# Kernel optimization log

Measured on AMD Instinct MI355X. Metric: run time of the kernel, lower is better.

## Reference

```python
import jax, jax.numpy as jnp
import numpy as np

NEG_BIG = -9.0e15


def masked_mean_softmax(idx):
    # softmax over a 0/-inf mask == uniform weights over positions where idx > 0
    logits = jnp.where(idx > 0, 1.0, NEG_BIG).astype(jnp.float32)
    return jax.nn.softmax(logits, axis=1)


def setup_inputs() -> dict:
    key = jax.random.key(0)
    ks = jax.random.split(key, 8)
    N_NODES, N_EDGES, EDGE_ARITY, NODE_DEG = 100000, 50000, 32, 16
    D_IN, D_OUT, TV = 128, 128, 128
    stdv = 1.0 / np.sqrt(D_IN)
    u = lambda k, shp: jax.random.uniform(k, shp, jnp.float32, -stdv, stdv)
    return {
        "x": jax.random.normal(ks[0], (N_NODES, D_IN), jnp.float32),
        "seq": jax.random.randint(ks[1], (N_EDGES, EDGE_ARITY), 0, N_NODES),
        "useq": jax.random.randint(ks[2], (N_NODES, NODE_DEG), 0, N_EDGES),
        "TextVector": jax.random.normal(ks[3], (TV,), jnp.float32),
        "weight1": u(ks[4], (D_IN, D_OUT)),
        "weight2": u(ks[5], (D_OUT, D_OUT)),
        "weight3": u(ks[6], (TV, TV)),
    }


def reference(x, seq, useq, TextVector, weight1, weight2, weight3):
    # NOTE: the torch module overwrites TextVector with weight3[0]; dropout is
    # a no-op in eval mode and is omitted here.
    tv = weight3[0]                                   # [TV]
    dot = weight3 @ tv                                # [TV]
    cos = dot / (jnp.linalg.norm(tv) * jnp.linalg.norm(weight3, axis=1))
    inter_nw = jnp.mean(cos)                          # scalar

    xw = (x @ weight1) * inter_nw                     # [N, D_OUT]

    nor = masked_mean_softmax(seq)                    # [E, A]
    adj_with_fea = xw[seq]                            # [E, A, D_OUT] gather
    edge = jnp.einsum('eac,ea->ec', adj_with_fea, nor)
    edge = jax.nn.relu(edge)
    e1 = edge @ weight2                               # [E, D_OUT]

    u_nor = masked_mean_softmax(useq)                 # [N, K]
    edge_adj = e1[useq]                               # [N, K, D_OUT] gather
    node = jnp.einsum('nkc,nk->nc', edge_adj, u_nor)  # [N, D_OUT]
    return node
```

## Files before the change

### kernel.cpp

```cpp
#include <hip/hip_runtime.h>
#include <hip/hip_fp16.h>

#define ND 100000
#define NE 50000
#define AR 32
#define DG 16
#define D  128

__global__ __launch_bounds__(128) void k_inter(const float* __restrict__ w3,
                                               float* __restrict__ inter_out) {
    int j = threadIdx.x;
    float dot = 0.f, sq = 0.f, sq0 = 0.f;
    #pragma unroll 8
    for (int k = 0; k < D; ++k) {
        float wj = w3[j * D + k];
        float w0 = w3[k];
        dot += wj * w0;
        sq  += wj * wj;
        sq0 += w0 * w0;
    }
    float cosj = dot / (sqrtf(sq0) * sqrtf(sq));
    __shared__ float red[128];
    red[j] = cosj;
    __syncthreads();
    if (j == 0) {
        float s = 0.f;
        for (int i = 0; i < 128; ++i) s += red[i];
        inter_out[0] = s / 128.f;
    }
}

__global__ __launch_bounds__(256) void k_xw(const float* __restrict__ x,
                                            const float* __restrict__ w1,
                                            const float* __restrict__ inter_p,
                                            __half* __restrict__ xwh) {
    __shared__ __half w1h[D * D];
    __shared__ float  xs[32 * D];
    int t = threadIdx.x;

    const float4* w1v4 = (const float4*)w1;
    #pragma unroll
    for (int i = 0; i < 16; ++i) {
        float4 v = w1v4[i * 256 + t];
        __half2* dh = (__half2*)&w1h[(i * 256 + t) * 4];
        dh[0] = __floats2half2_rn(v.x, v.y);
        dh[1] = __floats2half2_rn(v.z, v.w);
    }
    int rowbase = blockIdx.x * 32;
    const float4* xg = (const float4*)(x + (size_t)rowbase * D);
    float4* xs4 = (float4*)xs;
    #pragma unroll
    for (int i = 0; i < 4; ++i) xs4[i * 256 + t] = xg[i * 256 + t];
    __syncthreads();

    float inter = inter_p[0];
    int rg = t >> 5;
    int cg = t & 31;
    int r0 = rg * 4;
    int c0 = cg * 4;

    float acc[4][4] = {};
    #pragma unroll 4
    for (int k = 0; k < D; ++k) {
        float xv[4];
        #pragma unroll
        for (int i = 0; i < 4; ++i) xv[i] = xs[(r0 + i) * D + k];
        __half2 wa = *(const __half2*)&w1h[k * D + c0];
        __half2 wb = *(const __half2*)&w1h[k * D + c0 + 2];
        float wc0 = __low2float(wa), wc1 = __high2float(wa);
        float wc2 = __low2float(wb), wc3 = __high2float(wb);
        #pragma unroll
        for (int i = 0; i < 4; ++i) {
            acc[i][0] = fmaf(xv[i], wc0, acc[i][0]);
            acc[i][1] = fmaf(xv[i], wc1, acc[i][1]);
            acc[i][2] = fmaf(xv[i], wc2, acc[i][2]);
            acc[i][3] = fmaf(xv[i], wc3, acc[i][3]);
        }
    }
    #pragma unroll
    for (int i = 0; i < 4; ++i) {
        size_t r = (size_t)(rowbase + r0 + i);
        __half2* dst = (__half2*)(xwh + r * D + c0);
        dst[0] = __floats2half2_rn(acc[i][0] * inter, acc[i][1] * inter);
        dst[1] = __floats2half2_rn(acc[i][2] * inter, acc[i][3] * inter);
    }
}

__global__ __launch_bounds__(256) void k_edge(const int* __restrict__ seq,
                                              const __half* __restrict__ xwh,
                                              const float* __restrict__ w2,
                                              __half* __restrict__ e1h) {
    __shared__ __half w2h[D * D];
    __shared__ float  ebuf[8][D];
    int t = threadIdx.x;

    const float4* w2v4 = (const float4*)w2;
    #pragma unroll
    for (int i = 0; i < 16; ++i) {
        float4 v = w2v4[i * 256 + t];
        __half2* dh = (__half2*)&w2h[(i * 256 + t) * 4];
        dh[0] = __floats2half2_rn(v.x, v.y);
        dh[1] = __floats2half2_rn(v.z, v.w);
    }

    int wave = t >> 6;
    int lane = t & 63;
    int sub  = lane >> 5;
    int il   = lane & 31;
    int gw   = blockIdx.x * 4 + wave;
    int e    = gw * 2 + sub;

    int  sval  = seq[(size_t)e * AR + il];
    bool valid = sval > 0;
    unsigned long long b = __ballot(valid);
    int cnt = __popcll(sub ? (b >> 32) : (b & 0xffffffffULL));
    const float wuni = 1.f / 32.f;
    float wv = (cnt > 0) ? 1.f / (float)cnt : wuni;

    int c0 = il * 4;
    float a0 = 0.f, a1 = 0.f, a2 = 0.f, a3 = 0.f;
    #pragma unroll
    for (int a = 0; a < AR; ++a) {
        int srow = __shfl(sval, (sub << 5) + a, 64);
        float wa = (cnt > 0) ? ((srow > 0) ? wv : 0.f) : wuni;
        const __half2* p = (const __half2*)(xwh + (size_t)srow * D + c0);
        __half2 v01 = p[0], v23 = p[1];
        a0 = fmaf(wa, __low2float(v01),  a0);
        a1 = fmaf(wa, __high2float(v01), a1);
        a2 = fmaf(wa, __low2float(v23),  a2);
        a3 = fmaf(wa, __high2float(v23), a3);
    }
    float* eb = ebuf[wave * 2 + sub];
    eb[c0 + 0] = fmaxf(a0, 0.f);
    eb[c0 + 1] = fmaxf(a1, 0.f);
    eb[c0 + 2] = fmaxf(a2, 0.f);
    eb[c0 + 3] = fmaxf(a3, 0.f);
    __syncthreads();

    float o0 = 0.f, o1 = 0.f, o2 = 0.f, o3 = 0.f;
    #pragma unroll 4
    for (int c = 0; c < D; ++c) {
        float ec = eb[c];
        __half2 wa2 = *(const __half2*)&w2h[c * D + c0];
        __half2 wb2 = *(const __half2*)&w2h[c * D + c0 + 2];
        o0 = fmaf(ec, __low2float(wa2),  o0);
        o1 = fmaf(ec, __high2float(wa2), o1);
        o2 = fmaf(ec, __low2float(wb2),  o2);
        o3 = fmaf(ec, __high2float(wb2), o3);
    }
    __half2* dst = (__half2*)(e1h + (size_t)e * D + c0);
    dst[0] = __floats2half2_rn(o0, o1);
    dst[1] = __floats2half2_rn(o2, o3);
}

__global__ __launch_bounds__(256) void k_node(const int* __restrict__ useq,
                                              const __half* __restrict__ e1h,
                                              float* __restrict__ out) {
    int t = threadIdx.x;
    int wave = t >> 6, lane = t & 63;
    int n = blockIdx.x * 4 + wave;

    int  sval  = useq[(size_t)n * DG + (lane & 15)];
    bool valid = sval > 0;
    unsigned long long b = __ballot(valid);
    int cnt = __popcll(b & 0xFFFFULL);
    const float wuni = 1.f / 16.f;
    float wv = (cnt > 0) ? 1.f / (float)cnt : wuni;

    float a0 = 0.f, a1 = 0.f;
    #pragma unroll
    for (int k = 0; k < DG; ++k) {
        int srow = __shfl(sval, k, 64);
        float wa = (cnt > 0) ? ((srow > 0) ? wv : 0.f) : wuni;
        __half2 v = *(const __half2*)(e1h + (size_t)srow * D + lane * 2);
        a0 = fmaf(wa, __low2float(v),  a0);
        a1 = fmaf(wa, __high2float(v), a1);
    }
    float2* dst = (float2*)(out + (size_t)n * D + lane * 2);
    *dst = make_float2(a0, a1);
}

extern "C" void kernel_launch(void* const* d_in, const int* in_sizes, int n_in,
                              void* d_out, int out_size, void* d_ws, size_t ws_size,
                              hipStream_t stream) {
    const float* x    = (const float*)d_in[0];
    const int*   seq  = (const int*)d_in[1];
    const int*   useq = (const int*)d_in[2];
    const float* w1   = (const float*)d_in[4];
    const float* w2   = (const float*)d_in[5];
    const float* w3   = (const float*)d_in[6];
    float* out = (float*)d_out;

    __half* xwh   = (__half*)d_out;
    float*  inter = (float*)d_ws;
    __half* e1h   = (__half*)((char*)d_ws + 256);

    hipLaunchKernelGGL(k_inter, dim3(1),       dim3(128), 0, stream, w3, inter);
    hipLaunchKernelGGL(k_xw,    dim3(ND / 32), dim3(256), 0, stream, x, w1, inter, xwh);
    hipLaunchKernelGGL(k_edge,  dim3(NE / 8),  dim3(256), 0, stream, seq, xwh, w2, e1h);
    hipLaunchKernelGGL(k_node,  dim3(ND / 4),  dim3(256), 0, stream, useq, e1h, out);
}
```

Baseline: 269.2 us.

## Use MFMA f16 matrix cores for both dense GEMMs with pre-swizzled weight fragments

Adds a prep kernel that converts w1 and w2 to fp16 and lays them out in MFMA B-fragment order. The x@w1 and edge@w2 products now use mfma_f32_16x16x32_f16 instead of scalar FMA loops, with x also rounded to fp16 in padded shared memory. k_edge now handles 32 edges per block to feed the MFMA tiles. k_node is reworked to load 8 bytes per lane across two half-waves and combine them with a shuffle. This cuts ALU time in the GEMM stages and per-block weight conversion work, at the cost of extra fp16 rounding of x and of the edge activations.

```diff
diff --git a/kernel.cpp b/kernel.cpp
--- a/kernel.cpp
+++ b/kernel.cpp
@@ -6,6 +6,12 @@
 #define AR 32
 #define DG 16
 #define D  128
+
+typedef _Float16 half8_t __attribute__((ext_vector_type(8)));
+typedef _Float16 half4_t __attribute__((ext_vector_type(4)));
+typedef float    f32x4_t __attribute__((ext_vector_type(4)));
+
+#define APAD 136
 
 __global__ __launch_bounds__(128) void k_inter(const float* __restrict__ w3,
                                                float* __restrict__ inter_out) {
@@ -30,154 +36,185 @@
     }
 }
 
+__global__ __launch_bounds__(256) void k_prep(const float* __restrict__ w1,
+                                              const float* __restrict__ w2,
+                                              _Float16* __restrict__ w1f,
+                                              _Float16* __restrict__ w2f) {
+    int o = blockIdx.x * 256 + threadIdx.x;
+    int j    = o & 7;
+    int lane = (o >> 3) & 63;
+    int frag = o >> 9;
+    int ntile = frag >> 2, ktile = frag & 3;
+    int n = ntile * 16 + (lane & 15);
+    int k = ktile * 32 + (lane >> 4) * 8 + j;
+    w1f[o] = (_Float16)w1[k * D + n];
+    w2f[o] = (_Float16)w2[k * D + n];
+}
+
 __global__ __launch_bounds__(256) void k_xw(const float* __restrict__ x,
-                                            const float* __restrict__ w1,
+                                            const _Float16* __restrict__ w1f_g,
                                             const float* __restrict__ inter_p,
-                                            __half* __restrict__ xwh) {
-    __shared__ __half w1h[D * D];
-    __shared__ float  xs[32 * D];
+                                            _Float16* __restrict__ xwh) {
+    __shared__ _Float16 wfrag[D * D];
+    __shared__ _Float16 xs[64 * APAD];
     int t = threadIdx.x;
 
-    const float4* w1v4 = (const float4*)w1;
-    #pragma unroll
-    for (int i = 0; i < 16; ++i) {
-        float4 v = w1v4[i * 256 + t];
-        __half2* dh = (__half2*)&w1h[(i * 256 + t) * 4];
-        dh[0] = __floats2half2_rn(v.x, v.y);
-        dh[1] = __floats2half2_rn(v.z, v.w);
-    }
-    int rowbase = blockIdx.x * 32;
-    const float4* xg = (const float4*)(x + (size_t)rowbase * D);
-    float4* xs4 = (float4*)xs;
-    #pragma unroll
-    for (int i = 0; i < 4; ++i) xs4[i * 256 + t] = xg[i * 256 + t];
+    {
+        const float4* src = (const float4*)w1f_g;
+        float4* dst = (float4*)wfrag;
+        #pragma unroll
+        for (int i = 0; i < 8; ++i) dst[i * 256 + t] = src[i * 256 + t];
+    }
+    int rowbase = blockIdx.x * 64;
+    #pragma unroll
+    for (int p = 0; p < 8; ++p) {
+        int idx = p * 1024 + t * 4;
+        int r = idx >> 7, c = idx & 127;
+        int grow = rowbase + r;
+        float4 v = make_float4(0.f, 0.f, 0.f, 0.f);
+        if (grow < ND) v = ((const float4*)x)[(size_t)grow * 32 + (c >> 2)];
+        half4_t h = { (_Float16)v.x, (_Float16)v.y, (_Float16)v.z, (_Float16)v.w };
+        *(half4_t*)&xs[r * APAD + c] = h;
+    }
     __syncthreads();
 
+    int wave = t >> 6, lane = t & 63;
+    int quad = lane >> 4, l15 = lane & 15;
+    int m0 = wave * 16;
     float inter = inter_p[0];
-    int rg = t >> 5;
-    int cg = t & 31;
-    int r0 = rg * 4;
-    int c0 = cg * 4;
-
-    float acc[4][4] = {};
-    #pragma unroll 4
-    for (int k = 0; k < D; ++k) {
-        float xv[4];
-        #pragma unroll
-        for (int i = 0; i < 4; ++i) xv[i] = xs[(r0 + i) * D + k];
-        __half2 wa = *(const __half2*)&w1h[k * D + c0];
-        __half2 wb = *(const __half2*)&w1h[k * D + c0 + 2];
-        float wc0 = __low2float(wa), wc1 = __high2float(wa);
-        float wc2 = __low2float(wb), wc3 = __high2float(wb);
+
+    half8_t a[4];
+    #pragma unroll
+    for (int kt = 0; kt < 4; ++kt)
+        a[kt] = *(const half8_t*)&xs[(m0 + l15) * APAD + kt * 32 + quad * 8];
+
+    #pragma unroll
+    for (int nt = 0; nt < 8; ++nt) {
+        f32x4_t acc = {0.f, 0.f, 0.f, 0.f};
+        #pragma unroll
+        for (int kt = 0; kt < 4; ++kt) {
+            half8_t b = *(const half8_t*)&wfrag[((nt * 4 + kt) * 64 + lane) * 8];
+            acc = __builtin_amdgcn_mfma_f32_16x16x32_f16(a[kt], b, acc, 0, 0, 0);
+        }
+        int col = nt * 16 + l15;
         #pragma unroll
         for (int i = 0; i < 4; ++i) {
-            acc[i][0] = fmaf(xv[i], wc0, acc[i][0]);
-            acc[i][1] = fmaf(xv[i], wc1, acc[i][1]);
-            acc[i][2] = fmaf(xv[i], wc2, acc[i][2]);
-            acc[i][3] = fmaf(xv[i], wc3, acc[i][3]);
-        }
-    }
-    #pragma unroll
-    for (int i = 0; i < 4; ++i) {
-        size_t r = (size_t)(rowbase + r0 + i);
-        __half2* dst = (__half2*)(xwh + r * D + c0);
-        dst[0] = __floats2half2_rn(acc[i][0] * inter, acc[i][1] * inter);
-        dst[1] = __floats2half2_rn(acc[i][2] * inter, acc[i][3] * inter);
+            int grow = rowbase + m0 + quad * 4 + i;
+            if (grow < ND)
+                xwh[(size_t)grow * D + col] = (_Float16)(acc[i] * inter);
+        }
     }
 }
 
 __global__ __launch_bounds__(256) void k_edge(const int* __restrict__ seq,
-                                              const __half* __restrict__ xwh,
-                                              const float* __restrict__ w2,
-                                              __half* __restrict__ e1h) {
-    __shared__ __half w2h[D * D];
-    __shared__ float  ebuf[8][D];
+                                              const _Float16* __restrict__ xwh,
+                                              const _Float16* __restrict__ w2f_g,
+                                              _Float16* __restrict__ e1h) {
+    __shared__ _Float16 wfrag[D * D];
+    __shared__ _Float16 et[32 * APAD];
     int t = threadIdx.x;
-
-    const float4* w2v4 = (const float4*)w2;
-    #pragma unroll
-    for (int i = 0; i < 16; ++i) {
-        float4 v = w2v4[i * 256 + t];
-        __half2* dh = (__half2*)&w2h[(i * 256 + t) * 4];
-        dh[0] = __floats2half2_rn(v.x, v.y);
-        dh[1] = __floats2half2_rn(v.z, v.w);
-    }
-
-    int wave = t >> 6;
-    int lane = t & 63;
-    int sub  = lane >> 5;
-    int il   = lane & 31;
-    int gw   = blockIdx.x * 4 + wave;
-    int e    = gw * 2 + sub;
-
-    int  sval  = seq[(size_t)e * AR + il];
-    bool valid = sval > 0;
-    unsigned long long b = __ballot(valid);
-    int cnt = __popcll(sub ? (b >> 32) : (b & 0xffffffffULL));
-    const float wuni = 1.f / 32.f;
-    float wv = (cnt > 0) ? 1.f / (float)cnt : wuni;
-
-    int c0 = il * 4;
-    float a0 = 0.f, a1 = 0.f, a2 = 0.f, a3 = 0.f;
-    #pragma unroll
-    for (int a = 0; a < AR; ++a) {
-        int srow = __shfl(sval, (sub << 5) + a, 64);
-        float wa = (cnt > 0) ? ((srow > 0) ? wv : 0.f) : wuni;
-        const __half2* p = (const __half2*)(xwh + (size_t)srow * D + c0);
-        __half2 v01 = p[0], v23 = p[1];
-        a0 = fmaf(wa, __low2float(v01),  a0);
-        a1 = fmaf(wa, __high2float(v01), a1);
-        a2 = fmaf(wa, __low2float(v23),  a2);
-        a3 = fmaf(wa, __high2float(v23), a3);
-    }
-    float* eb = ebuf[wave * 2 + sub];
-    eb[c0 + 0] = fmaxf(a0, 0.f);
-    eb[c0 + 1] = fmaxf(a1, 0.f);
-    eb[c0 + 2] = fmaxf(a2, 0.f);
-    eb[c0 + 3] = fmaxf(a3, 0.f);
+    {
+        const float4* src = (const float4*)w2f_g;
+        float4* dst = (float4*)wfrag;
+        #pragma unroll
+        for (int i = 0; i < 8; ++i) dst[i * 256 + t] = src[i * 256 + t];
+    }
+
+    int wave = t >> 6, lane = t & 63;
+    int sub = lane >> 5, il = lane & 31;
+    int eb0 = blockIdx.x * 32;
+
+    #pragma unroll
+    for (int p = 0; p < 4; ++p) {
+        int erow = p * 8 + wave * 2 + sub;
+        int e = eb0 + erow;
+        int es = (e < NE) ? e : (NE - 1);
+        int sval = seq[(size_t)es * AR + il];
+        unsigned long long b = __ballot(sval > 0);
+        int cnt = __popcll(sub ? (unsigned long long)(b >> 32)
+                               : (b & 0xffffffffULL));
+        const float wuni = 1.f / 32.f;
+        float wv = (cnt > 0) ? 1.f / (float)cnt : wuni;
+        int c0 = il * 4;
+        float a0 = 0.f, a1 = 0.f, a2 = 0.f, a3 = 0.f;
+        #pragma unroll
+        for (int a = 0; a < AR; ++a) {
+            int srow = __shfl(sval, (sub << 5) + a, 64);
+            float wa = (cnt > 0) ? ((srow > 0) ? wv : 0.f) : wuni;
+            half4_t v = *(const half4_t*)(xwh + (size_t)srow * D + c0);
+            a0 = fmaf(wa, (float)v[0], a0);
+            a1 = fmaf(wa, (float)v[1], a1);
+            a2 = fmaf(wa, (float)v[2], a2);
+            a3 = fmaf(wa, (float)v[3], a3);
+        }
+        half4_t h = { (_Float16)fmaxf(a0, 0.f), (_Float16)fmaxf(a1, 0.f),
+                      (_Float16)fmaxf(a2, 0.f), (_Float16)fmaxf(a3, 0.f) };
+        *(half4_t*)&et[erow * APAD + c0] = h;
+    }
     __syncthreads();
 
-    float o0 = 0.f, o1 = 0.f, o2 = 0.f, o3 = 0.f;
-    #pragma unroll 4
-    for (int c = 0; c < D; ++c) {
-        float ec = eb[c];
-        __half2 wa2 = *(const __half2*)&w2h[c * D + c0];
-        __half2 wb2 = *(const __half2*)&w2h[c * D + c0 + 2];
-        o0 = fmaf(ec, __low2float(wa2),  o0);
-        o1 = fmaf(ec, __high2float(wa2), o1);
-        o2 = fmaf(ec, __low2float(wb2),  o2);
-        o3 = fmaf(ec, __high2float(wb2), o3);
-    }
-    __half2* dst = (__half2*)(e1h + (size_t)e * D + c0);
-    dst[0] = __floats2half2_rn(o0, o1);
-    dst[1] = __floats2half2_rn(o2, o3);
+    int quad = lane >> 4, l15 = lane & 15;
+    int m0 = (wave >> 1) * 16;
+    int ng = (wave & 1) * 4;
+
+    half8_t a[4];
+    #pragma unroll
+    for (int kt = 0; kt < 4; ++kt)
+        a[kt] = *(const half8_t*)&et[(m0 + l15) * APAD + kt * 32 + quad * 8];
+
+    #pragma unroll
+    for (int nt2 = 0; nt2 < 4; ++nt2) {
+        int nt = ng + nt2;
+        f32x4_t acc = {0.f, 0.f, 0.f, 0.f};
+        #pragma unroll
+        for (int kt = 0; kt < 4; ++kt) {
+            half8_t b = *(const half8_t*)&wfrag[((nt * 4 + kt) * 64 + lane) * 8];
+            acc = __builtin_amdgcn_mfma_f32_16x16x32_f16(a[kt], b, acc, 0, 0, 0);
+        }
+        int col = nt * 16 + l15;
+        #pragma unroll
+        for (int i = 0; i < 4; ++i) {
+            int e = eb0 + m0 + quad * 4 + i;
+            if (e < NE)
+                e1h[(size_t)e * D + col] = (_Float16)acc[i];
+        }
+    }
 }
 
 __global__ __launch_bounds__(256) void k_node(const int* __restrict__ useq,
-                                              const __half* __restrict__ e1h,
+                                              const _Float16* __restrict__ e1h,
                                               float* __restrict__ out) {
     int t = threadIdx.x;
     int wave = t >> 6, lane = t & 63;
     int n = blockIdx.x * 4 + wave;
-
-    int  sval  = useq[(size_t)n * DG + (lane & 15)];
-    bool valid = sval > 0;
-    unsigned long long b = __ballot(valid);
+    int hf = lane >> 5, il = lane & 31;
+
+    int sval = useq[(size_t)n * DG + (lane & 15)];
+    unsigned long long b = __ballot(sval > 0);
     int cnt = __popcll(b & 0xFFFFULL);
     const float wuni = 1.f / 16.f;
     float wv = (cnt > 0) ? 1.f / (float)cnt : wuni;
 
-    float a0 = 0.f, a1 = 0.f;
-    #pragma unroll
-    for (int k = 0; k < DG; ++k) {
+    float a0 = 0.f, a1 = 0.f, a2 = 0.f, a3 = 0.f;
+    #pragma unroll
+    for (int i = 0; i < 8; ++i) {
+        int k = i * 2 + hf;
         int srow = __shfl(sval, k, 64);
         float wa = (cnt > 0) ? ((srow > 0) ? wv : 0.f) : wuni;
-        __half2 v = *(const __half2*)(e1h + (size_t)srow * D + lane * 2);
-        a0 = fmaf(wa, __low2float(v),  a0);
-        a1 = fmaf(wa, __high2float(v), a1);
-    }
-    float2* dst = (float2*)(out + (size_t)n * D + lane * 2);
-    *dst = make_float2(a0, a1);
+        half4_t v = *(const half4_t*)(e1h + (size_t)srow * D + il * 4);
+        a0 = fmaf(wa, (float)v[0], a0);
+        a1 = fmaf(wa, (float)v[1], a1);
+        a2 = fmaf(wa, (float)v[2], a2);
+        a3 = fmaf(wa, (float)v[3], a3);
+    }
+    a0 += __shfl_down(a0, 32, 64);
+    a1 += __shfl_down(a1, 32, 64);
+    a2 += __shfl_down(a2, 32, 64);
+    a3 += __shfl_down(a3, 32, 64);
+    if (lane < 32) {
+        float4 o = make_float4(a0, a1, a2, a3);
+        ((float4*)(out + (size_t)n * D))[il] = o;
+    }
 }
 
 extern "C" void kernel_launch(void* const* d_in, const int* in_sizes, int n_in,
@@ -191,12 +228,15 @@
     const float* w3   = (const float*)d_in[6];
     float* out = (float*)d_out;
 
-    __half* xwh   = (__half*)d_out;
-    float*  inter = (float*)d_ws;
-    __half* e1h   = (__half*)((char*)d_ws + 256);
-
-    hipLaunchKernelGGL(k_inter, dim3(1),       dim3(128), 0, stream, w3, inter);
-    hipLaunchKernelGGL(k_xw,    dim3(ND / 32), dim3(256), 0, stream, x, w1, inter, xwh);
-    hipLaunchKernelGGL(k_edge,  dim3(NE / 8),  dim3(256), 0, stream, seq, xwh, w2, e1h);
-    hipLaunchKernelGGL(k_node,  dim3(ND / 4),  dim3(256), 0, stream, useq, e1h, out);
-}
+    _Float16* xwh   = (_Float16*)d_out;
+    float*    inter = (float*)d_ws;
+    _Float16* w1f   = (_Float16*)((char*)d_ws + 256);
+    _Float16* w2f   = (_Float16*)((char*)d_ws + 256 + 32768);
+    _Float16* e1h   = (_Float16*)((char*)d_ws + 256 + 65536);
+
+    hipLaunchKernelGGL(k_inter, dim3(1),              dim3(128), 0, stream, w3, inter);
+    hipLaunchKernelGGL(k_prep,  dim3(64),             dim3(256), 0, stream, w1, w2, w1f, w2f);
+    hipLaunchKernelGGL(k_xw,    dim3((ND + 63) / 64), dim3(256), 0, stream, x, w1f, inter, xwh);
+    hipLaunchKernelGGL(k_edge,  dim3((NE + 31) / 32), dim3(256), 0, stream, seq, xwh, w2f, e1h);
+    hipLaunchKernelGGL(k_node,  dim3(ND / 4),         dim3(256), 0, stream, useq, e1h, out);
+}
```

After: 230.3 us. -14.4%, faster.
